# Performance work log

Measured on AMD Instinct MI355X. Metric: run time of the kernel, lower is better.

Reference implementation:

```python
import jax, jax.numpy as jnp
import numpy as np

B, NS, NF, D, H = 64, 16, 4096, 128, 256  # batch, n_slots, n_feat, slot_dim, mlp_hidden
EPS_LN = 1e-5
EPS_ATT = 1e-8


def _layernorm(x, g, b):
    mu = x.mean(-1, keepdims=True)
    var = x.var(-1, keepdims=True)
    return (x - mu) / jnp.sqrt(var + EPS_LN) * g + b


def setup_inputs() -> dict:
    key = jax.random.key(0)
    ks = jax.random.split(key, 8)
    s = 0.02  # init scale for weights
    return {
        "t": jnp.zeros((), jnp.float32),
        "slots": jax.random.normal(ks[0], (B, NS, D), jnp.float32),
        "k": jax.random.normal(ks[1], (B, NF, D), jnp.float32),
        "v": jax.random.normal(ks[2], (B, NF, D), jnp.float32),
        "Wq": jax.random.normal(ks[3], (D, D), jnp.float32) * s,           # eqx Linear weight [out,in], no bias
        "ln_slots_g": jnp.ones((D,), jnp.float32),
        "ln_slots_b": jnp.zeros((D,), jnp.float32),
        "W_ih": jax.random.normal(ks[4], (3 * D, D), jnp.float32) * s,     # GRUCell input weights
        "W_hh": jax.random.normal(ks[5], (3 * D, D), jnp.float32) * s,     # GRUCell hidden weights
        "b_ih": jnp.zeros((3 * D,), jnp.float32),
        "b_n": jnp.zeros((D,), jnp.float32),
        "ln_ff_g": jnp.ones((D,), jnp.float32),
        "ln_ff_b": jnp.zeros((D,), jnp.float32),
        "W0": jax.random.normal(ks[6], (H, D), jnp.float32) * s,
        "b0": jnp.zeros((H,), jnp.float32),
        "W1": jax.random.normal(ks[7], (D, H), jnp.float32) * s,
        "b1": jnp.zeros((D,), jnp.float32),
    }


def reference(t, slots, k, v, Wq, ln_slots_g, ln_slots_b,
              W_ih, W_hh, b_ih, b_n, ln_ff_g, ln_ff_b, W0, b0, W1, b1):
    scale = D ** (-0.5)
    # LayerNorm over slot features, then query projection
    slots_norm = _layernorm(slots, ln_slots_g, ln_slots_b)
    q = jnp.einsum('bnd,ed->bne', slots_norm, Wq)                    # [B,NS,D]
    # Doubly-normalized slot attention: softmax over slots (axis=1), renorm over features
    att_logits = jnp.einsum('bnd,bmd->bnm', q, k) * scale            # [B,NS,NF]
    att = jax.nn.softmax(att_logits, axis=1)
    att = att / (att.sum(axis=-1, keepdims=True) + EPS_ATT)
    attended = jnp.einsum('bnm,bmd->bnd', att, v)                    # [B,NS,D]
    # GRUCell (equinox semantics): gates order (reset, input, new)
    igates = jnp.einsum('bnd,ed->bne', attended, W_ih) + b_ih        # [B,NS,3D]
    hgates = jnp.einsum('bnd,ed->bne', slots, W_hh)                  # [B,NS,3D]
    ir, ii, inew = jnp.split(igates, 3, axis=-1)
    hr, hi, hnew = jnp.split(hgates, 3, axis=-1)
    reset = jax.nn.sigmoid(ir + hr)
    inp = jax.nn.sigmoid(ii + hi)
    new = jnp.tanh(inew + reset * (hnew + b_n))
    gru_out = new + inp * (slots - new)                              # [B,NS,D]
    # LayerNorm -> MLP residual
    gru_normed = _layernorm(gru_out, ln_ff_g, ln_ff_b)
    h = jax.nn.relu(jnp.einsum('bnd,hd->bnh', gru_normed, W0) + b0)
    h = jnp.einsum('bnh,dh->bnd', h, W1) + b1
    target = gru_out + h
    return target - slots
```

## Files before the change

kernel.cpp:

```cpp
#include <hip/hip_runtime.h>
#include <hip/hip_bf16.h>
#include <math.h>

#define B_  64
#define NS_ 16
#define NF_ 4096
#define D_  128
#define H_  256


__device__ __forceinline__ float bflo(unsigned int u) { return __uint_as_float(u << 16); }
__device__ __forceinline__ float bfhi(unsigned int u) { return __uint_as_float(u & 0xffff0000u); }

__device__ __forceinline__ unsigned int pk_bf16(float a, float b) {
    unsigned int ua = __float_as_uint(a), ub = __float_as_uint(b);
    ua = (ua + 0x7FFFu + ((ua >> 16) & 1u)) >> 16;
    ub = (ub + 0x7FFFu + ((ub >> 16) & 1u)) >> 16;
    return ua | (ub << 16);
}

__device__ __forceinline__ float dot2_bf16(unsigned int a, unsigned int b, float c) {
    float d;
    asm("v_dot2_f32_bf16 %0, %1, %2, %3" : "=v"(d) : "v"(a), "v"(b), "v"(c));
    return d;
}

__device__ __forceinline__ float dot4(float4 a, float4 b) {
    return a.x * b.x + a.y * b.y + a.z * b.z + a.w * b.w;
}

__global__ __launch_bounds__(128) void k_q(
    const float* __restrict__ slots, const float* __restrict__ Wq,
    const float* __restrict__ lng, const float* __restrict__ lnb,
    unsigned int* __restrict__ q_out, float* __restrict__ acc, float* __restrict__ den) {
    const int b = blockIdx.x;
    const int t = threadIdx.x;
    __shared__ float sl_s[16][128];
    __shared__ float norm_s[16][128];
    __shared__ float st_s[16][8][2];
    __shared__ float mu_s[16], rs_s[16];
    __shared__ float q_s[16][128];

    const float4* sp = (const float4*)(slots + (size_t)b * 2048);
#pragma unroll
    for (int i = 0; i < 4; ++i) {
        int f = i * 128 + t;
        *(float4*)&sl_s[f >> 5][(f & 31) * 4] = sp[f];
    }
    __syncthreads();

    {
        int n = t >> 3, j = t & 7;
        float s1 = 0.f, s2 = 0.f;
#pragma unroll
        for (int d2 = 0; d2 < 16; ++d2) {
            float x = sl_s[n][j * 16 + d2];
            s1 += x; s2 += x * x;
        }
        st_s[n][j][0] = s1; st_s[n][j][1] = s2;
    }
    __syncthreads();
    if (t < 16) {
        float s1 = 0.f, s2 = 0.f;
#pragma unroll
        for (int j = 0; j < 8; ++j) { s1 += st_s[t][j][0]; s2 += st_s[t][j][1]; }
        float mu = s1 * (1.0f / 128.0f);
        float var = s2 * (1.0f / 128.0f) - mu * mu;
        mu_s[t] = mu;
        rs_s[t] = rsqrtf(var + 1e-5f);
    }
    __syncthreads();

    float gl = lng[t], bl = lnb[t];
#pragma unroll
    for (int n = 0; n < 16; ++n)
        norm_s[n][t] = (sl_s[n][t] - mu_s[n]) * rs_s[n] * gl + bl;
    __syncthreads();

    const float4* wq = (const float4*)(Wq + (size_t)t * 128);
    float qn[16];
#pragma unroll
    for (int n = 0; n < 16; ++n) qn[n] = 0.f;
#pragma unroll 4
    for (int j = 0; j < 32; ++j) {
        float4 w4 = wq[j];
#pragma unroll
        for (int n = 0; n < 16; ++n) qn[n] += dot4(w4, *(const float4*)&norm_s[n][4 * j]);
    }
#pragma unroll
    for (int n = 0; n < 16; ++n) q_s[n][t] = qn[n];

    float4 z4 = make_float4(0.f, 0.f, 0.f, 0.f);
    float4* ab = (float4*)(acc + (size_t)b * 2048);
#pragma unroll
    for (int i = 0; i < 4; ++i) ab[i * 128 + t] = z4;
    if (t < 16) den[b * 16 + t] = 0.f;
    __syncthreads();

    unsigned int* qo = q_out + (size_t)b * 1024;
#pragma unroll
    for (int i = 0; i < 8; ++i) {
        int u = i * 128 + t;
        int n = u >> 6, e2 = u & 63;
        qo[n * 64 + e2] = pk_bf16(q_s[n][2 * e2], q_s[n][2 * e2 + 1]);
    }
}

__global__ __launch_bounds__(256, 4) void k_attn(
    const float* __restrict__ kg_, const float* __restrict__ vg_,
    const unsigned int* __restrict__ q_u, float* __restrict__ acc_g, float* __restrict__ denom_g) {
    const int t = threadIdx.x;
    const int w = t >> 6, l = t & 63;
    const int b = blockIdx.y;
    const int n = l & 15;
    const int g = l >> 4;

    __shared__ unsigned int lds_u[6400];
    unsigned int* k_s = lds_u + w * 1344;
    float*        p_s = (float*)(k_s + 1088);

    uint4 qq[4];
    {
        const uint4* qrow = (const uint4*)q_u + ((b * 16 + n) * 16);
#pragma unroll
        for (int j = 0; j < 4; ++j) qq[j] = qrow[g * 4 + j];
    }

    float accL[16], accH[16];
#pragma unroll
    for (int i = 0; i < 16; ++i) { accL[i] = 0.f; accH[i] = 0.f; }
    float denom_acc = 0.f;

    const size_t mbase = (size_t)b * NF_ + blockIdx.x * 128 + w * 32;
    const float4* kg4 = (const float4*)kg_ + mbase * 32;
    const float2* vg2 = (const float2*)vg_ + mbase * 64;

    for (int tile = 0; tile < 2; ++tile) {
        const float4* kp = kg4 + tile * 512;
#pragma unroll
        for (int i = 0; i < 8; ++i) {
            float4 kk = kp[i * 64 + l];
            int off = (2 * i + (l >> 5)) * 68 + 2 * (l & 31);
            *(uint2*)&k_s[off] = make_uint2(pk_bf16(kk.x, kk.y), pk_bf16(kk.z, kk.w));
        }

#pragma unroll
        for (int mi = 0; mi < 16; ++mi) {
            float p0 = 0.f, p1 = 0.f, p2 = 0.f, p3 = 0.f;
#pragma unroll
            for (int j = 0; j < 4; ++j) {
                uint4 kk = *(const uint4*)&k_s[mi * 68 + g * 16 + 4 * j];
                p0 = dot2_bf16(kk.x, qq[j].x, p0);
                p1 = dot2_bf16(kk.y, qq[j].y, p1);
                p2 = dot2_bf16(kk.z, qq[j].z, p2);
                p3 = dot2_bf16(kk.w, qq[j].w, p3);
            }
            float x = (p0 + p1) + (p2 + p3);
            x += __shfl_xor(x, 16);
            x += __shfl_xor(x, 32);
            x *= 0.08838834764831845f;
            float e = __expf(x);
            float se = e;
            se += __shfl_xor(se, 1);
            se += __shfl_xor(se, 2);
            se += __shfl_xor(se, 4);
            se += __shfl_xor(se, 8);
            float pv = e * __builtin_amdgcn_rcpf(se);
            if (g == (mi & 3)) {
                denom_acc += pv;
                p_s[mi * 16 + n] = pv;
            }
        }

#pragma unroll
        for (int half = 0; half < 2; ++half) {
            float2 v2r[8];
#pragma unroll
            for (int i = 0; i < 8; ++i)
                v2r[i] = vg2[(size_t)(tile * 16 + half * 8 + i) * 64 + l];
#pragma unroll
            for (int i = 0; i < 8; ++i) {
                int mi = half * 8 + i;
                float vlo = v2r[i].x, vhi = v2r[i].y;
                float4 pp0 = *(const float4*)&p_s[mi * 16 + 0];
                float4 pp1 = *(const float4*)&p_s[mi * 16 + 4];
                float4 pp2 = *(const float4*)&p_s[mi * 16 + 8];
                float4 pp3 = *(const float4*)&p_s[mi * 16 + 12];
                accL[0]  = fmaf(pp0.x, vlo, accL[0]);  accH[0]  = fmaf(pp0.x, vhi, accH[0]);
                accL[1]  = fmaf(pp0.y, vlo, accL[1]);  accH[1]  = fmaf(pp0.y, vhi, accH[1]);
                accL[2]  = fmaf(pp0.z, vlo, accL[2]);  accH[2]  = fmaf(pp0.z, vhi, accH[2]);
                accL[3]  = fmaf(pp0.w, vlo, accL[3]);  accH[3]  = fmaf(pp0.w, vhi, accH[3]);
                accL[4]  = fmaf(pp1.x, vlo, accL[4]);  accH[4]  = fmaf(pp1.x, vhi, accH[4]);
                accL[5]  = fmaf(pp1.y, vlo, accL[5]);  accH[5]  = fmaf(pp1.y, vhi, accH[5]);
                accL[6]  = fmaf(pp1.z, vlo, accL[6]);  accH[6]  = fmaf(pp1.z, vhi, accH[6]);
                accL[7]  = fmaf(pp1.w, vlo, accL[7]);  accH[7]  = fmaf(pp1.w, vhi, accH[7]);
                accL[8]  = fmaf(pp2.x, vlo, accL[8]);  accH[8]  = fmaf(pp2.x, vhi, accH[8]);
                accL[9]  = fmaf(pp2.y, vlo, accL[9]);  accH[9]  = fmaf(pp2.y, vhi, accH[9]);
                accL[10] = fmaf(pp2.z, vlo, accL[10]); accH[10] = fmaf(pp2.z, vhi, accH[10]);
                accL[11] = fmaf(pp2.w, vlo, accL[11]); accH[11] = fmaf(pp2.w, vhi, accH[11]);
                accL[12] = fmaf(pp3.x, vlo, accL[12]); accH[12] = fmaf(pp3.x, vhi, accH[12]);
                accL[13] = fmaf(pp3.y, vlo, accL[13]); accH[13] = fmaf(pp3.y, vhi, accH[13]);
                accL[14] = fmaf(pp3.z, vlo, accL[14]); accH[14] = fmaf(pp3.z, vhi, accH[14]);
                accL[15] = fmaf(pp3.w, vlo, accL[15]); accH[15] = fmaf(pp3.w, vhi, accH[15]);
            }
        }
    }

    __syncthreads();
    float* red_f = (float*)lds_u;
    float* red_d = (float*)lds_u + 6144;
    red_d[t] = denom_acc;
    if (w > 0) {
#pragma unroll
        for (int nn = 0; nn < 16; ++nn)
            *(float2*)&red_f[(w - 1) * 2048 + nn * 128 + 2 * l] = make_float2(accL[nn], accH[nn]);
    }
    __syncthreads();
    if (w == 0) {
        float* base = acc_g + (size_t)(b * 16) * 128;
#pragma unroll
        for (int nn = 0; nn < 16; ++nn) {
            float2 r0 = *(const float2*)&red_f[0 * 2048 + nn * 128 + 2 * l];
            float2 r1 = *(const float2*)&red_f[1 * 2048 + nn * 128 + 2 * l];
            float2 r2 = *(const float2*)&red_f[2 * 2048 + nn * 128 + 2 * l];
            atomicAdd(base + nn * 128 + 2 * l,     accL[nn] + r0.x + r1.x + r2.x);
            atomicAdd(base + nn * 128 + 2 * l + 1, accH[nn] + r0.y + r1.y + r2.y);
        }
    }
    if (t < 16) {
        float s = 0.f;
#pragma unroll
        for (int j = 0; j < 16; ++j) s += red_d[t + 16 * j];
        atomicAdd(denom_g + b * 16 + t, s);
    }
}

__global__ __launch_bounds__(256) void k_final(
    const float* __restrict__ acc_g, const float* __restrict__ denom_g,
    const float* __restrict__ slots,
    const float* __restrict__ W_ih, const float* __restrict__ W_hh,
    const float* __restrict__ b_ih, const float* __restrict__ b_n,
    const float* __restrict__ ffg, const float* __restrict__ ffb,
    const float* __restrict__ W0, const float* __restrict__ b0,
    const float* __restrict__ W1, const float* __restrict__ b1,
    float* __restrict__ out) {
    const int bn0 = blockIdx.x * 4;
    const int t = threadIdx.x;
    __shared__ float att_s[4][128], slot_s[4][128];
    __shared__ float gates_s[4][4][128];
    __shared__ float gru_s[4][128], gn_s[4][128];
    __shared__ float h_s[4][256];

#pragma unroll
    for (int idx = t; idx < 512; idx += 256) {
        int bi = idx >> 7, d = idx & 127;
        int bn = bn0 + bi;
        float den = denom_g[bn] + 1e-8f;
        att_s[bi][d] = acc_g[(size_t)bn * 128 + d] / den;
        slot_s[bi][d] = slots[(size_t)bn * 128 + d];
    }
    __syncthreads();

    for (int g = t; g < 384; g += 256) {
        const float4* wi = (const float4*)(W_ih + (size_t)g * 128);
        const float4* wh = (const float4*)(W_hh + (size_t)g * 128);
        float si[4] = {0.f, 0.f, 0.f, 0.f}, sh[4] = {0.f, 0.f, 0.f, 0.f};
#pragma unroll 4
        for (int j = 0; j < 32; ++j) {
            float4 wi4 = wi[j], wh4 = wh[j];
#pragma unroll
            for (int bi = 0; bi < 4; ++bi) {
                si[bi] += dot4(wi4, *(const float4*)&att_s[bi][4 * j]);
                sh[bi] += dot4(wh4, *(const float4*)&slot_s[bi][4 * j]);
            }
        }
        float bih = b_ih[g];
        int d = g & 127;
#pragma unroll
        for (int bi = 0; bi < 4; ++bi) {
            if (g < 128)       gates_s[bi][0][d] = si[bi] + sh[bi] + bih;
            else if (g < 256)  gates_s[bi][1][d] = si[bi] + sh[bi] + bih;
            else { gates_s[bi][2][d] = si[bi] + bih; gates_s[bi][3][d] = sh[bi]; }
        }
    }
    __syncthreads();

    {
        int bi = t >> 6, l = t & 63;
        float gr[2], s1 = 0.f, s2 = 0.f;
#pragma unroll
        for (int h = 0; h < 2; ++h) {
            int d = l + 64 * h;
            float rr = 1.f / (1.f + __expf(-gates_s[bi][0][d]));
            float ii = 1.f / (1.f + __expf(-gates_s[bi][1][d]));
            float nv = tanhf(gates_s[bi][2][d] + rr * (gates_s[bi][3][d] + b_n[d]));
            float gru = nv + ii * (slot_s[bi][d] - nv);
            gr[h] = gru;
            gru_s[bi][d] = gru;
            s1 += gru; s2 += gru * gru;
        }
#pragma unroll
        for (int m = 1; m < 64; m <<= 1) { s1 += __shfl_xor(s1, m); s2 += __shfl_xor(s2, m); }
        float mu = s1 * (1.0f / 128.0f);
        float var = s2 * (1.0f / 128.0f) - mu * mu;
        float rstd = rsqrtf(var + 1e-5f);
#pragma unroll
        for (int h = 0; h < 2; ++h) {
            int d = l + 64 * h;
            gn_s[bi][d] = (gr[h] - mu) * rstd * ffg[d] + ffb[d];
        }
    }
    __syncthreads();

    {
        const float4* w0 = (const float4*)(W0 + (size_t)t * 128);
        float s[4] = {0.f, 0.f, 0.f, 0.f};
#pragma unroll 4
        for (int j = 0; j < 32; ++j) {
            float4 w4 = w0[j];
#pragma unroll
            for (int bi = 0; bi < 4; ++bi) s[bi] += dot4(w4, *(const float4*)&gn_s[bi][4 * j]);
        }
        float b0v = b0[t];
#pragma unroll
        for (int bi = 0; bi < 4; ++bi) h_s[bi][t] = fmaxf(s[bi] + b0v, 0.f);
    }
    __syncthreads();

    {
        int dr = t & 127, bp = (t >> 7) * 2;
        const float4* w1 = (const float4*)(W1 + (size_t)dr * 256);
        float s[2] = {0.f, 0.f};
#pragma unroll 4
        for (int j = 0; j < 64; ++j) {
            float4 w4 = w1[j];
#pragma unroll
            for (int u = 0; u < 2; ++u) s[u] += dot4(w4, *(const float4*)&h_s[bp + u][4 * j]);
        }
        float b1v = b1[dr];
#pragma unroll
        for (int u = 0; u < 2; ++u) {
            int bi = bp + u;
            out[(size_t)(bn0 + bi) * 128 + dr] = gru_s[bi][dr] + s[u] + b1v - slot_s[bi][dr];
        }
    }
}

extern "C" void kernel_launch(void* const* d_in, const int* in_sizes, int n_in,
                              void* d_out, int out_size, void* d_ws, size_t ws_size,
                              hipStream_t stream) {
    const float* slots = (const float*)d_in[1];
    const float* k     = (const float*)d_in[2];
    const float* v     = (const float*)d_in[3];
    const float* Wq    = (const float*)d_in[4];
    const float* lng   = (const float*)d_in[5];
    const float* lnb   = (const float*)d_in[6];
    const float* W_ih  = (const float*)d_in[7];
    const float* W_hh  = (const float*)d_in[8];
    const float* b_ih  = (const float*)d_in[9];
    const float* b_n   = (const float*)d_in[10];
    const float* ffg   = (const float*)d_in[11];
    const float* ffb   = (const float*)d_in[12];
    const float* W0    = (const float*)d_in[13];
    const float* b0    = (const float*)d_in[14];
    const float* W1    = (const float*)d_in[15];
    const float* b1    = (const float*)d_in[16];

    char* ws = (char*)d_ws;
    unsigned int* q_u = (unsigned int*)ws;
    float* acc = (float*)(ws + 262144);
    float* den = (float*)(ws + 786432);

    k_q<<<dim3(B_), dim3(128), 0, stream>>>(slots, Wq, lng, lnb, q_u, acc, den);
    k_attn<<<dim3(32, B_), dim3(256), 0, stream>>>(k, v, q_u, acc, den);
    k_final<<<dim3(256), dim3(256), 0, stream>>>(acc, den, slots, W_ih, W_hh,
                                                 b_ih, b_n, ffg, ffb, W0, b0, W1, b1,
                                                 (float*)d_out);
}
```

Before: 433.8 us.

## Share P across waves and split attn@V by feature column per thread

The attention kernel now has each wave compute probabilities for its own 16 rows of a shared 64-row tile, written to block-wide LDS. After a barrier, every thread accumulates a fixed feature column for 8 slots over all 64 rows. This removes the per-wave 16x128 partial accumulators and the cross-wave LDS reduction, cutting registers from 32 accumulators to 8 and reducing LDS use. In exchange it adds two block barriers per tile, uses strided scalar V loads that coalesce across threads, and drops the occupancy hint from launch bounds.

```diff
diff --git a/kernel.cpp b/kernel.cpp
--- a/kernel.cpp
+++ b/kernel.cpp
@@ -106,7 +106,7 @@
     }
 }
 
-__global__ __launch_bounds__(256, 4) void k_attn(
+__global__ __launch_bounds__(256) void k_attn(
     const float* __restrict__ kg_, const float* __restrict__ vg_,
     const unsigned int* __restrict__ q_u, float* __restrict__ acc_g, float* __restrict__ denom_g) {
     const int t = threadIdx.x;
@@ -114,10 +114,13 @@
     const int b = blockIdx.y;
     const int n = l & 15;
     const int g = l >> 4;
-
-    __shared__ unsigned int lds_u[6400];
-    unsigned int* k_s = lds_u + w * 1344;
-    float*        p_s = (float*)(k_s + 1088);
+    const int dcol = t & 127;
+    const int nh = t >> 7;
+
+    __shared__ unsigned int lds_u[5632];
+    unsigned int* k_s  = lds_u;
+    float*        p_s  = (float*)(lds_u + 4352);
+    float*        red_d = (float*)(lds_u + 5376);
 
     uint4 qq[4];
     {
@@ -126,30 +129,37 @@
         for (int j = 0; j < 4; ++j) qq[j] = qrow[g * 4 + j];
     }
 
-    float accL[16], accH[16];
-#pragma unroll
-    for (int i = 0; i < 16; ++i) { accL[i] = 0.f; accH[i] = 0.f; }
+    float acc[8];
+#pragma unroll
+    for (int i = 0; i < 8; ++i) acc[i] = 0.f;
     float denom_acc = 0.f;
 
-    const size_t mbase = (size_t)b * NF_ + blockIdx.x * 128 + w * 32;
-    const float4* kg4 = (const float4*)kg_ + mbase * 32;
-    const float2* vg2 = (const float2*)vg_ + mbase * 64;
+    const size_t mbase = (size_t)b * NF_ + blockIdx.x * 128;
+    const float4* kg4 = (const float4*)kg_ + (mbase + w * 16) * 32;
+    const float*  vgp = vg_ + mbase * 128 + dcol;
 
     for (int tile = 0; tile < 2; ++tile) {
-        const float4* kp = kg4 + tile * 512;
-#pragma unroll
-        for (int i = 0; i < 8; ++i) {
-            float4 kk = kp[i * 64 + l];
-            int off = (2 * i + (l >> 5)) * 68 + 2 * (l & 31);
-            *(uint2*)&k_s[off] = make_uint2(pk_bf16(kk.x, kk.y), pk_bf16(kk.z, kk.w));
+        const float4* kp = kg4 + tile * 64 * 32;
+#pragma unroll
+        for (int c = 0; c < 2; ++c) {
+            float4 tmp[4];
+#pragma unroll
+            for (int i = 0; i < 4; ++i) tmp[i] = kp[(c * 4 + i) * 64 + l];
+#pragma unroll
+            for (int i = 0; i < 4; ++i) {
+                int r = w * 16 + 2 * (c * 4 + i) + (l >> 5);
+                *(uint2*)&k_s[r * 68 + 2 * (l & 31)] =
+                    make_uint2(pk_bf16(tmp[i].x, tmp[i].y), pk_bf16(tmp[i].z, tmp[i].w));
+            }
         }
 
 #pragma unroll
         for (int mi = 0; mi < 16; ++mi) {
+            const int row = w * 16 + mi;
             float p0 = 0.f, p1 = 0.f, p2 = 0.f, p3 = 0.f;
 #pragma unroll
             for (int j = 0; j < 4; ++j) {
-                uint4 kk = *(const uint4*)&k_s[mi * 68 + g * 16 + 4 * j];
+                uint4 kk = *(const uint4*)&k_s[row * 68 + g * 16 + 4 * j];
                 p0 = dot2_bf16(kk.x, qq[j].x, p0);
                 p1 = dot2_bf16(kk.y, qq[j].y, p1);
                 p2 = dot2_bf16(kk.z, qq[j].z, p2);
@@ -168,65 +178,41 @@
             float pv = e * __builtin_amdgcn_rcpf(se);
             if (g == (mi & 3)) {
                 denom_acc += pv;
-                p_s[mi * 16 + n] = pv;
-            }
-        }
-
-#pragma unroll
-        for (int half = 0; half < 2; ++half) {
-            float2 v2r[8];
-#pragma unroll
-            for (int i = 0; i < 8; ++i)
-                v2r[i] = vg2[(size_t)(tile * 16 + half * 8 + i) * 64 + l];
+                p_s[row * 16 + n] = pv;
+            }
+        }
+        __syncthreads();
+
+        const float* vt = vgp + (size_t)tile * 64 * 128;
+#pragma unroll
+        for (int oct = 0; oct < 8; ++oct) {
+            float vv[8];
+#pragma unroll
+            for (int i = 0; i < 8; ++i) vv[i] = vt[(oct * 8 + i) * 128];
 #pragma unroll
             for (int i = 0; i < 8; ++i) {
-                int mi = half * 8 + i;
-                float vlo = v2r[i].x, vhi = v2r[i].y;
-                float4 pp0 = *(const float4*)&p_s[mi * 16 + 0];
-                float4 pp1 = *(const float4*)&p_s[mi * 16 + 4];
-                float4 pp2 = *(const float4*)&p_s[mi * 16 + 8];
-                float4 pp3 = *(const float4*)&p_s[mi * 16 + 12];
-                accL[0]  = fmaf(pp0.x, vlo, accL[0]);  accH[0]  = fmaf(pp0.x, vhi, accH[0]);
-                accL[1]  = fmaf(pp0.y, vlo, accL[1]);  accH[1]  = fmaf(pp0.y, vhi, accH[1]);
-                accL[2]  = fmaf(pp0.z, vlo, accL[2]);  accH[2]  = fmaf(pp0.z, vhi, accH[2]);
-                accL[3]  = fmaf(pp0.w, vlo, accL[3]);  accH[3]  = fmaf(pp0.w, vhi, accH[3]);
-                accL[4]  = fmaf(pp1.x, vlo, accL[4]);  accH[4]  = fmaf(pp1.x, vhi, accH[4]);
-                accL[5]  = fmaf(pp1.y, vlo, accL[5]);  accH[5]  = fmaf(pp1.y, vhi, accH[5]);
-                accL[6]  = fmaf(pp1.z, vlo, accL[6]);  accH[6]  = fmaf(pp1.z, vhi, accH[6]);
-                accL[7]  = fmaf(pp1.w, vlo, accL[7]);  accH[7]  = fmaf(pp1.w, vhi, accH[7]);
-                accL[8]  = fmaf(pp2.x, vlo, accL[8]);  accH[8]  = fmaf(pp2.x, vhi, accH[8]);
-                accL[9]  = fmaf(pp2.y, vlo, accL[9]);  accH[9]  = fmaf(pp2.y, vhi, accH[9]);
-                accL[10] = fmaf(pp2.z, vlo, accL[10]); accH[10] = fmaf(pp2.z, vhi, accH[10]);
-                accL[11] = fmaf(pp2.w, vlo, accL[11]); accH[11] = fmaf(pp2.w, vhi, accH[11]);
-                accL[12] = fmaf(pp3.x, vlo, accL[12]); accH[12] = fmaf(pp3.x, vhi, accH[12]);
-                accL[13] = fmaf(pp3.y, vlo, accL[13]); accH[13] = fmaf(pp3.y, vhi, accH[13]);
-                accL[14] = fmaf(pp3.z, vlo, accL[14]); accH[14] = fmaf(pp3.z, vhi, accH[14]);
-                accL[15] = fmaf(pp3.w, vlo, accL[15]); accH[15] = fmaf(pp3.w, vhi, accH[15]);
-            }
-        }
-    }
-
-    __syncthreads();
-    float* red_f = (float*)lds_u;
-    float* red_d = (float*)lds_u + 6144;
+                int m = oct * 8 + i;
+                float4 pa = *(const float4*)&p_s[m * 16 + nh * 8];
+                float4 pb = *(const float4*)&p_s[m * 16 + nh * 8 + 4];
+                acc[0] = fmaf(pa.x, vv[i], acc[0]);
+                acc[1] = fmaf(pa.y, vv[i], acc[1]);
+                acc[2] = fmaf(pa.z, vv[i], acc[2]);
+                acc[3] = fmaf(pa.w, vv[i], acc[3]);
+                acc[4] = fmaf(pb.x, vv[i], acc[4]);
+                acc[5] = fmaf(pb.y, vv[i], acc[5]);
+                acc[6] = fmaf(pb.z, vv[i], acc[6]);
+                acc[7] = fmaf(pb.w, vv[i], acc[7]);
+            }
+        }
+        __syncthreads();
+    }
+
     red_d[t] = denom_acc;
-    if (w > 0) {
-#pragma unroll
-        for (int nn = 0; nn < 16; ++nn)
-            *(float2*)&red_f[(w - 1) * 2048 + nn * 128 + 2 * l] = make_float2(accL[nn], accH[nn]);
-    }
-    __syncthreads();
-    if (w == 0) {
-        float* base = acc_g + (size_t)(b * 16) * 128;
-#pragma unroll
-        for (int nn = 0; nn < 16; ++nn) {
-            float2 r0 = *(const float2*)&red_f[0 * 2048 + nn * 128 + 2 * l];
-            float2 r1 = *(const float2*)&red_f[1 * 2048 + nn * 128 + 2 * l];
-            float2 r2 = *(const float2*)&red_f[2 * 2048 + nn * 128 + 2 * l];
-            atomicAdd(base + nn * 128 + 2 * l,     accL[nn] + r0.x + r1.x + r2.x);
-            atomicAdd(base + nn * 128 + 2 * l + 1, accH[nn] + r0.y + r1.y + r2.y);
-        }
-    }
+    __syncthreads();
+    float* base = acc_g + (size_t)b * 2048 + dcol;
+#pragma unroll
+    for (int i = 0; i < 8; ++i)
+        atomicAdd(base + (nh * 8 + i) * 128, acc[i]);
     if (t < 16) {
         float s = 0.f;
 #pragma unroll
```

After: 378.8 us. 1.15x faster.
